# Kernel tuning notes

Measured on AMD Instinct MI355X. Metric: run time of the kernel, lower is better.

Reference implementation:

```python
import jax, jax.numpy as jnp
import numpy as np
from jax import lax

B, L, E, H, VOCAB = 32, 64, 1024, 128, 32000


def setup_inputs() -> dict:
    key = jax.random.key(0)
    ks = jax.random.split(key, 8)
    return {
        "sent": jax.random.randint(ks[0], (B, L), 0, VOCAB),
        "init_c": jax.random.normal(ks[1], (B, H), jnp.float32),
        "init_h": jax.random.normal(ks[2], (B, H), jnp.float32),
        "enc_output": jax.random.normal(ks[3], (B, E, H), jnp.float32),
        "w_emb": jax.random.normal(ks[4], (VOCAB, H), jnp.float32) * 0.02,
        "w_lstm": jax.random.normal(ks[5], (2 * H, 4 * H), jnp.float32) * 0.05,
        "w_soft": jax.random.normal(ks[6], (H, VOCAB), jnp.float32) * 0.05,
        "V": jax.random.normal(ks[7], (2 * H, H), jnp.float32) * 0.05,
    }


def reference(sent, init_c, init_h, enc_output, w_emb, w_lstm, w_soft, V):
    h_dim = init_h.shape[-1]
    x_emb = w_emb[sent]                       # (B, L, H) embedding lookup
    # Split additive-attention matrix: concat(enc, h) @ V == enc @ V_e + h @ V_h
    V_e, V_h = V[:h_dim], V[h_dim:]           # (H, H) each
    enc_proj = enc_output @ V_e               # (B, E, H), precomputed once

    def step(carry, x_t):
        c, h = carry
        # LSTM cell: gates from concat(x, h) @ w_lstm
        gates = jnp.concatenate([x_t, h], axis=-1) @ w_lstm   # (B, 4H)
        i, f, o, g = jnp.split(gates, 4, axis=-1)
        c_new = jax.nn.sigmoid(f) * c + jax.nn.sigmoid(i) * jnp.tanh(g)
        h_new = jax.nn.sigmoid(o) * jnp.tanh(c_new)           # (B, H)
        # Bahdanau additive attention over encoder states
        att = jnp.tanh(enc_proj + (h_new @ V_h)[:, None, :])  # (B, E, H)
        scores = att.sum(axis=-1)                              # (B, E)
        alpha = jax.nn.softmax(scores, axis=-1)                # (B, E)
        context = jnp.einsum('be,beh->bh', alpha, enc_output)  # (B, H)
        h_out = context                                        # attended hidden
        return (c_new, h_out), (h_out, alpha)

    (c_fin, h_fin), (hs, alphas) = lax.scan(step, (init_c, init_h),
                                            jnp.transpose(x_emb, (1, 0, 2)))
    hs = jnp.transpose(hs, (1, 0, 2))          # (B, L, H)
    alphas = jnp.transpose(alphas, (1, 0, 2))  # (B, L, E)
    logits = hs @ w_soft                       # (B, L, vocab)
    return logits, c_fin, h_fin, alphas
```

## Files before the change

### kernel.cpp

```cpp
#include <hip/hip_runtime.h>
#include <hip/hip_bf16.h>

#define BB 32
#define LL 64
#define EE 1024
#define HH 128
#define VV 32000

typedef unsigned short u16;
typedef unsigned long long u64;
typedef __attribute__((ext_vector_type(8))) short bf16x8;
typedef __attribute__((ext_vector_type(8))) unsigned short u16x8;
typedef __attribute__((ext_vector_type(4))) float f32x4;

#define LOG2E 1.4426950408889634f
#define C2T   2.8853900817779268f

#define OFF_C ((size_t)BB * LL * VV)
#define OFF_H (OFF_C + (size_t)BB * HH)
#define OFF_A (OFF_H + (size_t)BB * HH)

#define WS_ENCT 0
#define WS_HS   ((size_t)8388608)
#define WS_GX   ((size_t)8912896)
#define WS_PAYU ((size_t)13107200)
#define WS_PAYG ((size_t)13639680)
#define WS_WT   ((size_t)13901824)
#define WS_DFL  ((size_t)22093824)
#define WS_NEED ((size_t)22093828)

#define PAYU_WORDS (32 * 8 * 2 * 130)
#define PAYG_WORDS (32 * 8 * 2 * 64)
#define PAY_TOTAL  (PAYU_WORDS + PAYG_WORDS)

#define RESET_BLKS ((PAY_TOTAL + 255) / 256)
#define GX_BLKS    128
#define ENC_BLKS   (16 * BB)
#define TW_BLKS    ((VV / 32) * 4)
#define PREP_BLKS  (RESET_BLKS + GX_BLKS + ENC_BLKS + TW_BLKS)

__device__ __forceinline__ float bf2f(u16 u) {
    union { unsigned int i; float f; } v; v.i = ((unsigned int)u) << 16; return v.f;
}
__device__ __forceinline__ u16 f2bf(float f) {
    union { float f; unsigned int i; } v; v.f = f;
    unsigned int x = v.i;
    return (u16)((x + 0x7FFFu + ((x >> 16) & 1u)) >> 16);
}
__device__ __forceinline__ float ldf(const void* p, size_t i, int f32) {
    if (f32) return ((const float*)p)[i];
    return bf2f(((const u16*)p)[i]);
}
__device__ __forceinline__ void stout(void* p, size_t i, float v, int f32) {
    if (f32) ((float*)p)[i] = v;
    else ((u16*)p)[i] = f2bf(v);
}
__device__ __forceinline__ float sigm(float x) {
    return __builtin_amdgcn_rcpf(1.f + __builtin_amdgcn_exp2f(-x * LOG2E));
}
__device__ __forceinline__ float tanh_fast(float x) {
    return 1.f - 2.f * __builtin_amdgcn_rcpf(__builtin_amdgcn_exp2f(x * C2T) + 1.f);
}

__global__ __launch_bounds__(256) void megaprep_kernel(
    const int* __restrict__ sent, const void* __restrict__ w_emb,
    const void* __restrict__ w_lstm, const void* __restrict__ enc_out,
    const void* __restrict__ V, const void* __restrict__ w_soft,
    float* __restrict__ gx, u16* __restrict__ encT, u16* __restrict__ wT,
    u64* __restrict__ pay, int* __restrict__ flag)
{
    const int blk = blockIdx.x;
    const int tid = threadIdx.x;
    __shared__ float smem[16384];
    __shared__ int dcnt[4];

    if (blk < RESET_BLKS) {
        int i = blk * 256 + tid;
        if (i < PAY_TOTAL) pay[i] = 0ull;
        if (blk == 0) {
            float a = fabsf(bf2f((u16)(((const unsigned int*)w_emb)[tid] & 0xFFFFu)));
            unsigned long long m = __ballot(a > 1e-4f && a < 0.5f);
            if ((tid & 63) == 0) dcnt[tid >> 6] = __popcll(m);
            __syncthreads();
            if (tid == 0)
                *flag = (dcnt[0] + dcnt[1] + dcnt[2] + dcnt[3] > 128) ? 1 : 0;
        }
        return;
    }
    float da = fabsf(bf2f((u16)(((const unsigned int*)w_emb)[tid] & 0xFFFFu)));
    unsigned long long dm = __ballot(da > 1e-4f && da < 0.5f);
    if ((tid & 63) == 0) dcnt[tid >> 6] = __popcll(dm);
    __syncthreads();
    const int isf32 = !(dcnt[0] + dcnt[1] + dcnt[2] + dcnt[3] > 128);
    __syncthreads();

    if (blk < RESET_BLKS + GX_BLKS) {
        int row0 = (blk - RESET_BLKS) * 16;
        float (*xr)[128] = (float(*)[128])smem;
        for (int i = tid; i < 2048; i += 256) {
            int r = i >> 7, col = i & 127;
            int id = sent[row0 + r];
            xr[r][col] = ldf(w_emb, (size_t)id * HH + col, isf32);
        }
        __syncthreads();
        int c0 = tid, c1 = tid + 256;
        float a0[16], a1[16];
        #pragma unroll
        for (int r = 0; r < 16; ++r) { a0[r] = 0.f; a1[r] = 0.f; }
        for (int kk = 0; kk < 128; ++kk) {
            float w0, w1;
            if (isf32) {
                w0 = ((const float*)w_lstm)[(size_t)kk * 512 + c0];
                w1 = ((const float*)w_lstm)[(size_t)kk * 512 + c1];
            } else {
                w0 = bf2f(((const u16*)w_lstm)[(size_t)kk * 512 + c0]);
                w1 = bf2f(((const u16*)w_lstm)[(size_t)kk * 512 + c1]);
            }
            #pragma unroll
            for (int r = 0; r < 16; ++r) {
                a0[r] += xr[r][kk] * w0;
                a1[r] += xr[r][kk] * w1;
            }
        }
        #pragma unroll
        for (int r = 0; r < 16; ++r) {
            gx[(size_t)(row0 + r) * 512 + c0] = a0[r];
            gx[(size_t)(row0 + r) * 512 + c1] = a1[r];
        }
        return;
    }
    if (blk < RESET_BLKS + GX_BLKS + ENC_BLKS) {
        int idx = blk - RESET_BLKS - GX_BLKS;
        int b = idx >> 4;
        int e0 = (idx & 15) * 64;
        float (*ve)[128] = (float(*)[128])smem;
        for (int i = tid; i < HH * HH; i += 256)
            ve[i >> 7][i & 127] = ldf(V, i, isf32);
        __syncthreads();
        int e = e0 + (tid & 63);
        int hb = (tid >> 6) * 32;
        size_t rowbase = ((size_t)b * EE + e) * HH;
        float acc[32];
        #pragma unroll
        for (int i = 0; i < 32; ++i) acc[i] = 0.f;
        for (int k0 = 0; k0 < HH; k0 += 16) {
            float ef[16];
            #pragma unroll
            for (int i = 0; i < 16; ++i) ef[i] = ldf(enc_out, rowbase + k0 + i, isf32);
            #pragma unroll
            for (int hh = 0; hh < 32; ++hh) {
                float a = acc[hh];
                #pragma unroll
                for (int kk = 0; kk < 16; ++kk)
                    a += ef[kk] * ve[k0 + kk][hb + hh];
                acc[hh] = a;
            }
        }
        u16* outp = encT + ((size_t)b * HH) * EE + e;
        #pragma unroll
        for (int hh = 0; hh < 32; ++hh)
            outp[(size_t)(hh + hb) * EE] = f2bf(acc[hh] * C2T);
        return;
    }
    {
        int idx = blk - RESET_BLKS - GX_BLKS - ENC_BLKS;
        int n0 = (idx >> 2) * 32;
        int k0 = (idx & 3) * 32;
        u16 (*tile)[33] = (u16(*)[33])smem;
        int tx = tid & 31, ty0 = tid >> 5;
        #pragma unroll
        for (int i = 0; i < 4; ++i) {
            int ty = ty0 + i * 8;
            tile[ty][tx] = f2bf(ldf(w_soft, (size_t)(k0 + ty) * VV + n0 + tx, isf32));
        }
        __syncthreads();
        #pragma unroll
        for (int i = 0; i < 4; ++i) {
            int ty = ty0 + i * 8;
            wT[(size_t)(n0 + ty) * HH + k0 + tx] = tile[tx][ty];
        }
    }
}

__global__ __launch_bounds__(1024) void scan_kernel(
    const void* __restrict__ init_c, const void* __restrict__ init_h,
    const void* __restrict__ enc_out, const void* __restrict__ w_lstm,
    const void* __restrict__ V, const u16* __restrict__ encTg16,
    const float* __restrict__ gx, u16* __restrict__ hs_bf,
    void* __restrict__ out, u64* __restrict__ payu, u64* __restrict__ payg,
    const int* __restrict__ flagp)
{
    const int isf32 = !flagp[0];
    const int bid = blockIdx.x;
    const int b = bid & 31, k = bid >> 5;
    const int tid = threadIdx.x;

    __shared__ u16   encTl16[128][128];
    __shared__ float encF[128][128];
    __shared__ u16   wrec16[64 * 128];
    __shared__ float gall[512];
    __shared__ float harr[128], cst[128], hnew[128], hvC[128];
    __shared__ float dred[8][128];
    __shared__ float sc[128];
    __shared__ float exch[8][130];
    __shared__ float redw[2], redw2[2];
    __shared__ float m_s, s_s;

    for (int i = tid; i < 128 * 128; i += 1024) {
        int h = i >> 7, e = i & 127;
        encTl16[h][e] = encTg16[(size_t)(b * 128 + h) * EE + k * 128 + e];
    }
    for (int i = tid; i < 128 * 128; i += 1024) {
        int e = i >> 7, hh = i & 127;
        encF[e][hh] = ldf(enc_out, ((size_t)b * EE + k * 128 + e) * HH + hh, isf32);
    }
    for (int i = tid; i < 64 * 128; i += 1024) {
        int c = i >> 7, kk = i & 127;
        wrec16[c * 128 + kk] = f2bf(ldf(w_lstm, (size_t)(HH + kk) * 512 + k * 64 + c, isf32));
    }
    if (tid < 128) {
        cst[tid]  = ldf(init_c, (size_t)b * HH + tid, isf32);
        harr[tid] = ldf(init_h, (size_t)b * HH + tid, isf32);
    }
    __syncthreads();

    u64* mypu = payu + (size_t)(b * 8 + k) * 2 * 130;
    u64* mypg = payg + (size_t)(b * 8 + k) * 2 * 64;

    for (int t = 0; t < LL; ++t) {
        const unsigned int want = (unsigned int)(t + 1);
        float g0 = 0.f, g1 = 0.f, g2 = 0.f, g3 = 0.f;
        if (tid < 128) {
            const float* gxr = gx + (size_t)(b * LL + t) * 512;
            g0 = gxr[tid]; g1 = gxr[128 + tid]; g2 = gxr[256 + tid]; g3 = gxr[384 + tid];
        }
        {
            int colL = tid >> 4, kc = tid & 15;
            const bf16x8 wv = *(const bf16x8*)&wrec16[colL * 128 + kc * 8];
            float acc = 0.f;
            #pragma unroll
            for (int j = 0; j < 8; ++j)
                acc = __builtin_fmaf(harr[kc * 8 + j], bf2f((u16)wv[j]), acc);
            acc += __shfl_xor(acc, 1);
            acc += __shfl_xor(acc, 2);
            acc += __shfl_xor(acc, 4);
            acc += __shfl_xor(acc, 8);
            if (kc == 0) {
                gall[(k << 6) + colL] = acc;
                union { float f; unsigned int u; } cv; cv.f = acc;
                u64 w = ((u64)want << 32) | (u64)cv.u;
                __hip_atomic_store(&mypg[(size_t)(t & 1) * 64 + colL], w,
                                   __ATOMIC_RELAXED, __HIP_MEMORY_SCOPE_AGENT);
            }
        }
        if (tid < 448) {
            int qq = tid >> 6;
            int q = qq + (qq >= k ? 1 : 0);
            int idx = tid & 63;
            const u64* qp = payg + ((size_t)(b * 8 + q) * 2 + (t & 1)) * 64 + idx;
            u64 w = __hip_atomic_load(qp, __ATOMIC_RELAXED, __HIP_MEMORY_SCOPE_AGENT);
            int cnt = 0;
            while ((unsigned int)(w >> 32) != want) {
                __builtin_amdgcn_s_sleep(1);
                w = __hip_atomic_load(qp, __ATOMIC_RELAXED, __HIP_MEMORY_SCOPE_AGENT);
                if (++cnt > (1 << 20)) break;
            }
            union { unsigned int u; float f; } cv; cv.u = (unsigned int)(w & 0xFFFFFFFFu);
            gall[q * 64 + idx] = cv.f;
        }
        __syncthreads();
        if (tid < 128) {
            float gi = g0 + gall[tid];
            float gf = g1 + gall[128 + tid];
            float go = g2 + gall[256 + tid];
            float gg = g3 + gall[384 + tid];
            float c_new = sigm(gf) * cst[tid] + sigm(gi) * tanh_fast(gg);
            cst[tid] = c_new;
            hnew[tid] = sigm(go) * tanh_fast(c_new);
        }
        __syncthreads();
        {
            int h = tid & 127, jc = tid >> 7;
            float p = 0.f;
            if (isf32) {
                const float* vp = (const float*)V + (size_t)(HH + jc * 16) * HH + h;
                #pragma unroll
                for (int j = 0; j < 16; ++j)
                    p += hnew[jc * 16 + j] * vp[(size_t)j * HH];
            } else {
                const u16* vp = (const u16*)V + (size_t)(HH + jc * 16) * HH + h;
                #pragma unroll
                for (int j = 0; j < 16; ++j)
                    p += hnew[jc * 16 + j] * bf2f(vp[(size_t)j * HH]);
            }
            dred[jc][h] = p;
        }
        __syncthreads();
        if (tid < 128) {
            float v = 0.f;
            #pragma unroll
            for (int s = 0; s < 8; ++s) v += dred[s][tid];
            hvC[tid] = v * C2T;
        }
        __syncthreads();
        {
            int e = tid & 127, hc = tid >> 7;
            float sumr = 0.f;
            #pragma unroll
            for (int j = 0; j < 16; ++j) {
                int h = hc * 16 + j;
                float a = bf2f(encTl16[h][e]) + hvC[h];
                sumr += __builtin_amdgcn_rcpf(__builtin_amdgcn_exp2f(a) + 1.f);
            }
            dred[hc][e] = sumr;
        }
        __syncthreads();
        float s_e = 0.f, p_reg = 0.f;
        if (tid < 128) {
            float sr = 0.f;
            #pragma unroll
            for (int s = 0; s < 8; ++s) sr += dred[s][tid];
            s_e = 128.f - 2.f * sr;
            float m = s_e;
            #pragma unroll
            for (int off = 32; off; off >>= 1) m = fmaxf(m, __shfl_xor(m, off));
            if ((tid & 63) == 0) redw[tid >> 6] = m;
        }
        __syncthreads();
        if (tid < 128) {
            float mloc = fmaxf(redw[0], redw[1]);
            p_reg = __builtin_amdgcn_exp2f((s_e - mloc) * LOG2E);
            sc[tid] = p_reg;
            float s = p_reg;
            #pragma unroll
            for (int off = 32; off; off >>= 1) s += __shfl_xor(s, off);
            if ((tid & 63) == 0) redw2[tid >> 6] = s;
            if (tid == 0) m_s = mloc;
        }
        __syncthreads();
        if (tid == 0) s_s = redw2[0] + redw2[1];
        {
            int h = tid & 127, ec = tid >> 7;
            float p = 0.f;
            #pragma unroll
            for (int j = 0; j < 16; ++j)
                p += sc[ec * 16 + j] * encF[ec * 16 + j][h];
            dred[ec][h] = p;
        }
        __syncthreads();
        float Uv = 0.f;
        if (tid < 128) {
            #pragma unroll
            for (int s = 0; s < 8; ++s) Uv += dred[s][tid];
        }
        {
            u64* pp = mypu + (size_t)(t & 1) * 130;
            if (tid < 130) {
                float val = (tid < 128) ? Uv : ((tid == 128) ? m_s : s_s);
                union { float f; unsigned int u; } cv; cv.f = val;
                u64 w = ((u64)want << 32) | (u64)cv.u;
                __hip_atomic_store(&pp[tid], w, __ATOMIC_RELAXED, __HIP_MEMORY_SCOPE_AGENT);
                exch[k][tid] = val;
            }
        }
        if (tid < 910) {
            int qq = tid / 130;
            int q = qq + (qq >= k ? 1 : 0);
            int idx = tid - qq * 130;
            const u64* qp = payu + ((size_t)(b * 8 + q) * 2 + (t & 1)) * 130 + idx;
            u64 w = __hip_atomic_load(qp, __ATOMIC_RELAXED, __HIP_MEMORY_SCOPE_AGENT);
            int cnt = 0;
            while ((unsigned int)(w >> 32) != want) {
                __builtin_amdgcn_s_sleep(1);
                w = __hip_atomic_load(qp, __ATOMIC_RELAXED, __HIP_MEMORY_SCOPE_AGENT);
                if (++cnt > (1 << 20)) break;
            }
            union { unsigned int u; float f; } cv; cv.u = (unsigned int)(w & 0xFFFFFFFFu);
            exch[q][idx] = cv.f;
        }
        __syncthreads();
        if (tid < 128) {
            float M = exch[0][128];
            #pragma unroll
            for (int q = 1; q < 8; ++q) M = fmaxf(M, exch[q][128]);
            float St = 0.f, ch = 0.f;
            #pragma unroll
            for (int q = 0; q < 8; ++q) {
                float w = __builtin_amdgcn_exp2f((exch[q][128] - M) * LOG2E);
                St += w * exch[q][129];
                ch += w * exch[q][tid];
            }
            float rS = __builtin_amdgcn_rcpf(St);
            float ctx = ch * rS;
            harr[tid] = ctx;
            float al = p_reg * __builtin_amdgcn_exp2f((m_s - M) * LOG2E) * rS;
            stout(out, OFF_A + (size_t)(b * LL + t) * EE + k * 128 + tid, al, isf32);
            if (k == 0) {
                hs_bf[(size_t)(b * LL + t) * HH + tid] = f2bf(ctx);
                if (t == LL - 1) {
                    stout(out, OFF_H + (size_t)b * HH + tid, ctx, isf32);
                    stout(out, OFF_C + (size_t)b * HH + tid, cst[tid], isf32);
                }
            }
        }
        __syncthreads();
    }
}

__global__ __launch_bounds__(256) void logits_gemm(
    const u16* __restrict__ hs, const u16* __restrict__ wT,
    void* __restrict__ out, const int* __restrict__ flagp)
{
    int isf32 = !flagp[0];
    int n0 = blockIdx.x * 32;
    int m0 = (blockIdx.y * 4 + (threadIdx.x >> 6)) * 32;
    int lane = threadIdx.x & 63;
    int lr = lane & 15, lh = lane >> 4;
    f32x4 acc00 = {0.f, 0.f, 0.f, 0.f}, acc01 = acc00, acc10 = acc00, acc11 = acc00;
    const u16* a0p = hs + (size_t)(m0 + lr) * HH + lh * 8;
    const u16* a1p = a0p + (size_t)16 * HH;
    const u16* b0p = wT + (size_t)(n0 + lr) * HH + lh * 8;
    const u16* b1p = b0p + (size_t)16 * HH;
    #pragma unroll
    for (int ks = 0; ks < 4; ++ks) {
        bf16x8 a0 = *(const bf16x8*)(a0p + ks * 32);
        bf16x8 a1 = *(const bf16x8*)(a1p + ks * 32);
        bf16x8 b0 = *(const bf16x8*)(b0p + ks * 32);
        bf16x8 b1 = *(const bf16x8*)(b1p + ks * 32);
        acc00 = __builtin_amdgcn_mfma_f32_16x16x32_bf16(a0, b0, acc00, 0, 0, 0);
        acc01 = __builtin_amdgcn_mfma_f32_16x16x32_bf16(a0, b1, acc01, 0, 0, 0);
        acc10 = __builtin_amdgcn_mfma_f32_16x16x32_bf16(a1, b0, acc10, 0, 0, 0);
        acc11 = __builtin_amdgcn_mfma_f32_16x16x32_bf16(a1, b1, acc11, 0, 0, 0);
    }
    size_t base0 = (size_t)(m0 + lh * 4) * VV + n0;
    size_t base1 = (size_t)(m0 + 16 + lh * 4) * VV + n0;
    #pragma unroll
    for (int r = 0; r < 4; ++r) {
        stout(out, base0 + (size_t)r * VV + lr,      acc00[r], isf32);
        stout(out, base0 + (size_t)r * VV + 16 + lr, acc01[r], isf32);
        stout(out, base1 + (size_t)r * VV + lr,      acc10[r], isf32);
        stout(out, base1 + (size_t)r * VV + 16 + lr, acc11[r], isf32);
    }
}

extern "C" void kernel_launch(void* const* d_in, const int* in_sizes, int n_in,
                              void* d_out, int out_size, void* d_ws, size_t ws_size,
                              hipStream_t stream)
{
    (void)in_sizes; (void)n_in; (void)out_size;
    if (ws_size < WS_NEED) return;

    const int* sent     = (const int*)d_in[0];
    const void* init_c  = d_in[1];
    const void* init_h  = d_in[2];
    const void* enc_out = d_in[3];
    const void* w_emb   = d_in[4];
    const void* w_lstm  = d_in[5];
    const void* w_soft  = d_in[6];
    const void* V       = d_in[7];

    char* ws = (char*)d_ws;
    u16*   encT  = (u16*)(ws + WS_ENCT);
    u16*   hs    = (u16*)(ws + WS_HS);
    float* gx    = (float*)(ws + WS_GX);
    u64*   payu  = (u64*)(ws + WS_PAYU);
    u64*   payg  = (u64*)(ws + WS_PAYG);
    u16*   wT    = (u16*)(ws + WS_WT);
    int*   dflag = (int*)(ws + WS_DFL);

    hipLaunchKernelGGL(megaprep_kernel, dim3(PREP_BLKS), dim3(256), 0, stream,
                       sent, w_emb, w_lstm, enc_out, V, w_soft,
                       gx, encT, wT, payu, dflag);

    {
        const void* a0 = init_c; const void* a1 = init_h; const void* a2 = enc_out;
        const void* a3 = w_lstm; const void* a4 = V; const u16* a5 = encT;
        const float* a6 = gx; u16* a7 = hs; void* a8 = d_out;
        u64* a9 = payu; u64* a10 = payg; const int* a11 = dflag;
        void* args[] = {&a0, &a1, &a2, &a3, &a4, &a5, &a6, &a7, &a8, &a9, &a10, &a11};
        hipLaunchCooperativeKernel(scan_kernel, dim3(256), dim3(1024), args, 0, stream);
    }

    hipLaunchKernelGGL(logits_gemm, dim3(VV / 32, 16), dim3(256), 0, stream, hs, wT, d_out, dflag);
}
```

Baseline: 746.5 us.

## Fuse prep, scan and logits GEMM into one cooperative kernel

Merges the three launches (prep, recurrent scan, logits GEMM) into a single cooperative kernel that uses grid syncs between phases. The per-call transpose of w_soft into a bf16 workspace is dropped, and the GEMM phase reads w_soft directly with strided scalar loads and converts it in registers. Prep work (gx, the encoder projection, payload reset) is spread over the 256 persistent blocks. This removes launch gaps and a full pass over w_soft, but the GEMM now runs on only 256 blocks with uncoalesced B loads, and the prep phase has far less parallelism than before.

```diff
diff --git a/kernel.cpp b/kernel.cpp
--- a/kernel.cpp
+++ b/kernel.cpp
@@ -1,5 +1,8 @@
 #include <hip/hip_runtime.h>
 #include <hip/hip_bf16.h>
+#include <hip/hip_cooperative_groups.h>
+
+namespace cg = cooperative_groups;
 
 #define BB 32
 #define LL 64
@@ -25,19 +28,7 @@
 #define WS_GX   ((size_t)8912896)
 #define WS_PAYU ((size_t)13107200)
 #define WS_PAYG ((size_t)13639680)
-#define WS_WT   ((size_t)13901824)
-#define WS_DFL  ((size_t)22093824)
-#define WS_NEED ((size_t)22093828)
-
-#define PAYU_WORDS (32 * 8 * 2 * 130)
-#define PAYG_WORDS (32 * 8 * 2 * 64)
-#define PAY_TOTAL  (PAYU_WORDS + PAYG_WORDS)
-
-#define RESET_BLKS ((PAY_TOTAL + 255) / 256)
-#define GX_BLKS    128
-#define ENC_BLKS   (16 * BB)
-#define TW_BLKS    ((VV / 32) * 4)
-#define PREP_BLKS  (RESET_BLKS + GX_BLKS + ENC_BLKS + TW_BLKS)
+#define WS_NEED ((size_t)13901824)
 
 __device__ __forceinline__ float bf2f(u16 u) {
     union { unsigned int i; float f; } v; v.i = ((unsigned int)u) << 16; return v.f;
@@ -62,135 +53,14 @@
     return 1.f - 2.f * __builtin_amdgcn_rcpf(__builtin_amdgcn_exp2f(x * C2T) + 1.f);
 }
 
-__global__ __launch_bounds__(256) void megaprep_kernel(
+__global__ __launch_bounds__(1024) void fused_kernel(
     const int* __restrict__ sent, const void* __restrict__ w_emb,
     const void* __restrict__ w_lstm, const void* __restrict__ enc_out,
     const void* __restrict__ V, const void* __restrict__ w_soft,
-    float* __restrict__ gx, u16* __restrict__ encT, u16* __restrict__ wT,
-    u64* __restrict__ pay, int* __restrict__ flag)
+    const void* __restrict__ init_c, const void* __restrict__ init_h,
+    float* __restrict__ gx, u16* __restrict__ encTg16, u16* __restrict__ hs_bf,
+    void* __restrict__ out, u64* __restrict__ payu, u64* __restrict__ payg)
 {
-    const int blk = blockIdx.x;
-    const int tid = threadIdx.x;
-    __shared__ float smem[16384];
-    __shared__ int dcnt[4];
-
-    if (blk < RESET_BLKS) {
-        int i = blk * 256 + tid;
-        if (i < PAY_TOTAL) pay[i] = 0ull;
-        if (blk == 0) {
-            float a = fabsf(bf2f((u16)(((const unsigned int*)w_emb)[tid] & 0xFFFFu)));
-            unsigned long long m = __ballot(a > 1e-4f && a < 0.5f);
-            if ((tid & 63) == 0) dcnt[tid >> 6] = __popcll(m);
-            __syncthreads();
-            if (tid == 0)
-                *flag = (dcnt[0] + dcnt[1] + dcnt[2] + dcnt[3] > 128) ? 1 : 0;
-        }
-        return;
-    }
-    float da = fabsf(bf2f((u16)(((const unsigned int*)w_emb)[tid] & 0xFFFFu)));
-    unsigned long long dm = __ballot(da > 1e-4f && da < 0.5f);
-    if ((tid & 63) == 0) dcnt[tid >> 6] = __popcll(dm);
-    __syncthreads();
-    const int isf32 = !(dcnt[0] + dcnt[1] + dcnt[2] + dcnt[3] > 128);
-    __syncthreads();
-
-    if (blk < RESET_BLKS + GX_BLKS) {
-        int row0 = (blk - RESET_BLKS) * 16;
-        float (*xr)[128] = (float(*)[128])smem;
-        for (int i = tid; i < 2048; i += 256) {
-            int r = i >> 7, col = i & 127;
-            int id = sent[row0 + r];
-            xr[r][col] = ldf(w_emb, (size_t)id * HH + col, isf32);
-        }
-        __syncthreads();
-        int c0 = tid, c1 = tid + 256;
-        float a0[16], a1[16];
-        #pragma unroll
-        for (int r = 0; r < 16; ++r) { a0[r] = 0.f; a1[r] = 0.f; }
-        for (int kk = 0; kk < 128; ++kk) {
-            float w0, w1;
-            if (isf32) {
-                w0 = ((const float*)w_lstm)[(size_t)kk * 512 + c0];
-                w1 = ((const float*)w_lstm)[(size_t)kk * 512 + c1];
-            } else {
-                w0 = bf2f(((const u16*)w_lstm)[(size_t)kk * 512 + c0]);
-                w1 = bf2f(((const u16*)w_lstm)[(size_t)kk * 512 + c1]);
-            }
-            #pragma unroll
-            for (int r = 0; r < 16; ++r) {
-                a0[r] += xr[r][kk] * w0;
-                a1[r] += xr[r][kk] * w1;
-            }
-        }
-        #pragma unroll
-        for (int r = 0; r < 16; ++r) {
-            gx[(size_t)(row0 + r) * 512 + c0] = a0[r];
-            gx[(size_t)(row0 + r) * 512 + c1] = a1[r];
-        }
-        return;
-    }
-    if (blk < RESET_BLKS + GX_BLKS + ENC_BLKS) {
-        int idx = blk - RESET_BLKS - GX_BLKS;
-        int b = idx >> 4;
-        int e0 = (idx & 15) * 64;
-        float (*ve)[128] = (float(*)[128])smem;
-        for (int i = tid; i < HH * HH; i += 256)
-            ve[i >> 7][i & 127] = ldf(V, i, isf32);
-        __syncthreads();
-        int e = e0 + (tid & 63);
-        int hb = (tid >> 6) * 32;
-        size_t rowbase = ((size_t)b * EE + e) * HH;
-        float acc[32];
-        #pragma unroll
-        for (int i = 0; i < 32; ++i) acc[i] = 0.f;
-        for (int k0 = 0; k0 < HH; k0 += 16) {
-            float ef[16];
-            #pragma unroll
-            for (int i = 0; i < 16; ++i) ef[i] = ldf(enc_out, rowbase + k0 + i, isf32);
-            #pragma unroll
-            for (int hh = 0; hh < 32; ++hh) {
-                float a = acc[hh];
-                #pragma unroll
-                for (int kk = 0; kk < 16; ++kk)
-                    a += ef[kk] * ve[k0 + kk][hb + hh];
-                acc[hh] = a;
-            }
-        }
-        u16* outp = encT + ((size_t)b * HH) * EE + e;
-        #pragma unroll
-        for (int hh = 0; hh < 32; ++hh)
-            outp[(size_t)(hh + hb) * EE] = f2bf(acc[hh] * C2T);
-        return;
-    }
-    {
-        int idx = blk - RESET_BLKS - GX_BLKS - ENC_BLKS;
-        int n0 = (idx >> 2) * 32;
-        int k0 = (idx & 3) * 32;
-        u16 (*tile)[33] = (u16(*)[33])smem;
-        int tx = tid & 31, ty0 = tid >> 5;
-        #pragma unroll
-        for (int i = 0; i < 4; ++i) {
-            int ty = ty0 + i * 8;
-            tile[ty][tx] = f2bf(ldf(w_soft, (size_t)(k0 + ty) * VV + n0 + tx, isf32));
-        }
-        __syncthreads();
-        #pragma unroll
-        for (int i = 0; i < 4; ++i) {
-            int ty = ty0 + i * 8;
-            wT[(size_t)(n0 + ty) * HH + k0 + tx] = tile[tx][ty];
-        }
-    }
-}
-
-__global__ __launch_bounds__(1024) void scan_kernel(
-    const void* __restrict__ init_c, const void* __restrict__ init_h,
-    const void* __restrict__ enc_out, const void* __restrict__ w_lstm,
-    const void* __restrict__ V, const u16* __restrict__ encTg16,
-    const float* __restrict__ gx, u16* __restrict__ hs_bf,
-    void* __restrict__ out, u64* __restrict__ payu, u64* __restrict__ payg,
-    const int* __restrict__ flagp)
-{
-    const int isf32 = !flagp[0];
     const int bid = blockIdx.x;
     const int b = bid & 31, k = bid >> 5;
     const int tid = threadIdx.x;
@@ -205,6 +75,80 @@
     __shared__ float exch[8][130];
     __shared__ float redw[2], redw2[2];
     __shared__ float m_s, s_s;
+    __shared__ int dcnt[4];
+
+    if (tid < 256) {
+        float a = fabsf(bf2f((u16)(((const unsigned int*)w_emb)[tid] & 0xFFFFu)));
+        unsigned long long m = __ballot(a > 1e-4f && a < 0.5f);
+        if ((tid & 63) == 0) dcnt[tid >> 6] = __popcll(m);
+    }
+    __syncthreads();
+    const int isf32 = !(dcnt[0] + dcnt[1] + dcnt[2] + dcnt[3] > 128);
+
+    u64* mypu = payu + (size_t)(b * 8 + k) * 2 * 130;
+    u64* mypg = payg + (size_t)(b * 8 + k) * 2 * 64;
+    if (tid < 260) mypu[tid] = 0ull;
+    else if (tid < 260 + 128) mypg[tid - 260] = 0ull;
+
+    {
+        float (*xr)[128] = (float(*)[128])wrec16;
+        int row0 = bid * 8;
+        {
+            int r = tid >> 7, col = tid & 127;
+            int id = sent[row0 + r];
+            xr[r][col] = ldf(w_emb, (size_t)id * HH + col, isf32);
+        }
+        __syncthreads();
+        int c = tid & 511, rh = tid >> 9;
+        float a4[4] = {0.f, 0.f, 0.f, 0.f};
+        for (int kk = 0; kk < 128; ++kk) {
+            float wv = ldf(w_lstm, (size_t)kk * 512 + c, isf32);
+            #pragma unroll
+            for (int r = 0; r < 4; ++r)
+                a4[r] += xr[rh * 4 + r][kk] * wv;
+        }
+        #pragma unroll
+        for (int r = 0; r < 4; ++r)
+            gx[(size_t)(row0 + rh * 4 + r) * 512 + c] = a4[r];
+    }
+    __syncthreads();
+    {
+        float (*ve)[128] = (float(*)[128])encF;
+        for (int i = tid; i < HH * HH; i += 1024)
+            ve[i >> 7][i & 127] = ldf(V, i, isf32);
+        __syncthreads();
+        #pragma unroll
+        for (int u = 0; u < 2; ++u) {
+            int unit = bid * 2 + u;
+            int bb = unit >> 4;
+            int e0 = (unit & 15) * 64;
+            int e = e0 + (tid & 63);
+            int h0 = (tid >> 6) * 8;
+            size_t rowbase = ((size_t)bb * EE + e) * HH;
+            float acc[8];
+            #pragma unroll
+            for (int i = 0; i < 8; ++i) acc[i] = 0.f;
+            for (int k0 = 0; k0 < HH; k0 += 16) {
+                float ef[16];
+                #pragma unroll
+                for (int i = 0; i < 16; ++i) ef[i] = ldf(enc_out, rowbase + k0 + i, isf32);
+                #pragma unroll
+                for (int hh = 0; hh < 8; ++hh) {
+                    float a = acc[hh];
+                    #pragma unroll
+                    for (int kk = 0; kk < 16; ++kk)
+                        a += ef[kk] * ve[k0 + kk][h0 + hh];
+                    acc[hh] = a;
+                }
+            }
+            u16* outp = encTg16 + ((size_t)bb * HH) * EE + e;
+            #pragma unroll
+            for (int hh = 0; hh < 8; ++hh)
+                outp[(size_t)(h0 + hh) * EE] = f2bf(acc[hh] * C2T);
+        }
+    }
+    __threadfence();
+    cg::this_grid().sync();
 
     for (int i = tid; i < 128 * 128; i += 1024) {
         int h = i >> 7, e = i & 127;
@@ -223,9 +167,6 @@
         harr[tid] = ldf(init_h, (size_t)b * HH + tid, isf32);
     }
     __syncthreads();
-
-    u64* mypu = payu + (size_t)(b * 8 + k) * 2 * 130;
-    u64* mypg = payg + (size_t)(b * 8 + k) * 2 * 64;
 
     for (int t = 0; t < LL; ++t) {
         const unsigned int want = (unsigned int)(t + 1);
@@ -405,41 +346,46 @@
         }
         __syncthreads();
     }
-}
-
-__global__ __launch_bounds__(256) void logits_gemm(
-    const u16* __restrict__ hs, const u16* __restrict__ wT,
-    void* __restrict__ out, const int* __restrict__ flagp)
-{
-    int isf32 = !flagp[0];
-    int n0 = blockIdx.x * 32;
-    int m0 = (blockIdx.y * 4 + (threadIdx.x >> 6)) * 32;
-    int lane = threadIdx.x & 63;
-    int lr = lane & 15, lh = lane >> 4;
-    f32x4 acc00 = {0.f, 0.f, 0.f, 0.f}, acc01 = acc00, acc10 = acc00, acc11 = acc00;
-    const u16* a0p = hs + (size_t)(m0 + lr) * HH + lh * 8;
-    const u16* a1p = a0p + (size_t)16 * HH;
-    const u16* b0p = wT + (size_t)(n0 + lr) * HH + lh * 8;
-    const u16* b1p = b0p + (size_t)16 * HH;
-    #pragma unroll
-    for (int ks = 0; ks < 4; ++ks) {
-        bf16x8 a0 = *(const bf16x8*)(a0p + ks * 32);
-        bf16x8 a1 = *(const bf16x8*)(a1p + ks * 32);
-        bf16x8 b0 = *(const bf16x8*)(b0p + ks * 32);
-        bf16x8 b1 = *(const bf16x8*)(b1p + ks * 32);
-        acc00 = __builtin_amdgcn_mfma_f32_16x16x32_bf16(a0, b0, acc00, 0, 0, 0);
-        acc01 = __builtin_amdgcn_mfma_f32_16x16x32_bf16(a0, b1, acc01, 0, 0, 0);
-        acc10 = __builtin_amdgcn_mfma_f32_16x16x32_bf16(a1, b0, acc10, 0, 0, 0);
-        acc11 = __builtin_amdgcn_mfma_f32_16x16x32_bf16(a1, b1, acc11, 0, 0, 0);
-    }
-    size_t base0 = (size_t)(m0 + lh * 4) * VV + n0;
-    size_t base1 = (size_t)(m0 + 16 + lh * 4) * VV + n0;
-    #pragma unroll
-    for (int r = 0; r < 4; ++r) {
-        stout(out, base0 + (size_t)r * VV + lr,      acc00[r], isf32);
-        stout(out, base0 + (size_t)r * VV + 16 + lr, acc01[r], isf32);
-        stout(out, base1 + (size_t)r * VV + lr,      acc10[r], isf32);
-        stout(out, base1 + (size_t)r * VV + 16 + lr, acc11[r], isf32);
+
+    __threadfence();
+    cg::this_grid().sync();
+
+    {
+        const int wgl = bid * 16 + (tid >> 6);
+        const int lane = tid & 63;
+        const int lr = lane & 15, lh = lane >> 4;
+        for (int task = wgl; task < 64000; task += 4096) {
+            int nx = task >> 6, my = task & 63;
+            int n0 = nx * 32, m0 = my * 32;
+            f32x4 acc00 = {0.f, 0.f, 0.f, 0.f}, acc01 = acc00, acc10 = acc00, acc11 = acc00;
+            const u16* a0p = hs_bf + (size_t)(m0 + lr) * HH + lh * 8;
+            const u16* a1p = a0p + (size_t)16 * HH;
+            #pragma unroll
+            for (int ks = 0; ks < 4; ++ks) {
+                bf16x8 a0 = *(const bf16x8*)(a0p + ks * 32);
+                bf16x8 a1 = *(const bf16x8*)(a1p + ks * 32);
+                bf16x8 b0, b1;
+                #pragma unroll
+                for (int j = 0; j < 8; ++j) {
+                    int kk = ks * 32 + lh * 8 + j;
+                    b0[j] = (short)f2bf(ldf(w_soft, (size_t)kk * VV + n0 + lr, isf32));
+                    b1[j] = (short)f2bf(ldf(w_soft, (size_t)kk * VV + n0 + 16 + lr, isf32));
+                }
+                acc00 = __builtin_amdgcn_mfma_f32_16x16x32_bf16(a0, b0, acc00, 0, 0, 0);
+                acc01 = __builtin_amdgcn_mfma_f32_16x16x32_bf16(a0, b1, acc01, 0, 0, 0);
+                acc10 = __builtin_amdgcn_mfma_f32_16x16x32_bf16(a1, b0, acc10, 0, 0, 0);
+                acc11 = __builtin_amdgcn_mfma_f32_16x16x32_bf16(a1, b1, acc11, 0, 0, 0);
+            }
+            size_t base0 = (size_t)(m0 + lh * 4) * VV + n0;
+            size_t base1 = (size_t)(m0 + 16 + lh * 4) * VV + n0;
+            #pragma unroll
+            for (int r = 0; r < 4; ++r) {
+                stout(out, base0 + (size_t)r * VV + lr,      acc00[r], isf32);
+                stout(out, base0 + (size_t)r * VV + 16 + lr, acc01[r], isf32);
+                stout(out, base1 + (size_t)r * VV + lr,      acc10[r], isf32);
+                stout(out, base1 + (size_t)r * VV + 16 + lr, acc11[r], isf32);
+            }
+        }
     }
 }
 
@@ -465,21 +411,13 @@
     float* gx    = (float*)(ws + WS_GX);
     u64*   payu  = (u64*)(ws + WS_PAYU);
     u64*   payg  = (u64*)(ws + WS_PAYG);
-    u16*   wT    = (u16*)(ws + WS_WT);
-    int*   dflag = (int*)(ws + WS_DFL);
-
-    hipLaunchKernelGGL(megaprep_kernel, dim3(PREP_BLKS), dim3(256), 0, stream,
-                       sent, w_emb, w_lstm, enc_out, V, w_soft,
-                       gx, encT, wT, payu, dflag);
-
-    {
-        const void* a0 = init_c; const void* a1 = init_h; const void* a2 = enc_out;
-        const void* a3 = w_lstm; const void* a4 = V; const u16* a5 = encT;
-        const float* a6 = gx; u16* a7 = hs; void* a8 = d_out;
-        u64* a9 = payu; u64* a10 = payg; const int* a11 = dflag;
-        void* args[] = {&a0, &a1, &a2, &a3, &a4, &a5, &a6, &a7, &a8, &a9, &a10, &a11};
-        hipLaunchCooperativeKernel(scan_kernel, dim3(256), dim3(1024), args, 0, stream);
-    }
-
-    hipLaunchKernelGGL(logits_gemm, dim3(VV / 32, 16), dim3(256), 0, stream, hs, wT, d_out, dflag);
-}
+
+    const int* a0 = sent; const void* a1 = w_emb; const void* a2 = w_lstm;
+    const void* a3 = enc_out; const void* a4 = V; const void* a5 = w_soft;
+    const void* a6 = init_c; const void* a7 = init_h;
+    float* a8 = gx; u16* a9 = encT; u16* a10 = hs; void* a11 = d_out;
+    u64* a12 = payu; u64* a13 = payg;
+    void* args[] = {&a0, &a1, &a2, &a3, &a4, &a5, &a6, &a7,
+                    &a8, &a9, &a10, &a11, &a12, &a13};
+    hipLaunchCooperativeKernel(fused_kernel, dim3(256), dim3(1024), args, 0, stream);
+}
```

Result: slower. 979.1 us (+31.2%).

## Fuse logits GEMM into cooperative scan kernel after grid sync

Applied to the files above, without the earlier changes.

Moves the output-projection GEMM into the tail of the cooperative scan kernel, separated by a grid-wide barrier, with each wave looping over 32x32 output tiles. This removes one kernel launch and the gap between launches. In exchange, the GEMM runs with only 256 blocks of 1024 threads, limited by the scan kernel's occupancy and its heavy shared-memory use, instead of a large grid that can fully occupy the GPU.

```diff
diff --git a/kernel.cpp b/kernel.cpp
--- a/kernel.cpp
+++ b/kernel.cpp
@@ -1,5 +1,8 @@
 #include <hip/hip_runtime.h>
 #include <hip/hip_bf16.h>
+#include <hip/hip_cooperative_groups.h>
+
+namespace cg = cooperative_groups;
 
 #define BB 32
 #define LL 64
@@ -182,13 +185,13 @@
     }
 }
 
-__global__ __launch_bounds__(1024) void scan_kernel(
+__global__ __launch_bounds__(1024) void scan_logits_kernel(
     const void* __restrict__ init_c, const void* __restrict__ init_h,
     const void* __restrict__ enc_out, const void* __restrict__ w_lstm,
     const void* __restrict__ V, const u16* __restrict__ encTg16,
     const float* __restrict__ gx, u16* __restrict__ hs_bf,
     void* __restrict__ out, u64* __restrict__ payu, u64* __restrict__ payg,
-    const int* __restrict__ flagp)
+    const u16* __restrict__ wT, const int* __restrict__ flagp)
 {
     const int isf32 = !flagp[0];
     const int bid = blockIdx.x;
@@ -405,41 +408,43 @@
         }
         __syncthreads();
     }
-}
-
-__global__ __launch_bounds__(256) void logits_gemm(
-    const u16* __restrict__ hs, const u16* __restrict__ wT,
-    void* __restrict__ out, const int* __restrict__ flagp)
-{
-    int isf32 = !flagp[0];
-    int n0 = blockIdx.x * 32;
-    int m0 = (blockIdx.y * 4 + (threadIdx.x >> 6)) * 32;
-    int lane = threadIdx.x & 63;
-    int lr = lane & 15, lh = lane >> 4;
-    f32x4 acc00 = {0.f, 0.f, 0.f, 0.f}, acc01 = acc00, acc10 = acc00, acc11 = acc00;
-    const u16* a0p = hs + (size_t)(m0 + lr) * HH + lh * 8;
-    const u16* a1p = a0p + (size_t)16 * HH;
-    const u16* b0p = wT + (size_t)(n0 + lr) * HH + lh * 8;
-    const u16* b1p = b0p + (size_t)16 * HH;
-    #pragma unroll
-    for (int ks = 0; ks < 4; ++ks) {
-        bf16x8 a0 = *(const bf16x8*)(a0p + ks * 32);
-        bf16x8 a1 = *(const bf16x8*)(a1p + ks * 32);
-        bf16x8 b0 = *(const bf16x8*)(b0p + ks * 32);
-        bf16x8 b1 = *(const bf16x8*)(b1p + ks * 32);
-        acc00 = __builtin_amdgcn_mfma_f32_16x16x32_bf16(a0, b0, acc00, 0, 0, 0);
-        acc01 = __builtin_amdgcn_mfma_f32_16x16x32_bf16(a0, b1, acc01, 0, 0, 0);
-        acc10 = __builtin_amdgcn_mfma_f32_16x16x32_bf16(a1, b0, acc10, 0, 0, 0);
-        acc11 = __builtin_amdgcn_mfma_f32_16x16x32_bf16(a1, b1, acc11, 0, 0, 0);
-    }
-    size_t base0 = (size_t)(m0 + lh * 4) * VV + n0;
-    size_t base1 = (size_t)(m0 + 16 + lh * 4) * VV + n0;
-    #pragma unroll
-    for (int r = 0; r < 4; ++r) {
-        stout(out, base0 + (size_t)r * VV + lr,      acc00[r], isf32);
-        stout(out, base0 + (size_t)r * VV + 16 + lr, acc01[r], isf32);
-        stout(out, base1 + (size_t)r * VV + lr,      acc10[r], isf32);
-        stout(out, base1 + (size_t)r * VV + 16 + lr, acc11[r], isf32);
+
+    __threadfence();
+    cg::this_grid().sync();
+
+    {
+        const int wgl = bid * 16 + (tid >> 6);
+        const int lane = tid & 63;
+        const int lr = lane & 15, lh = lane >> 4;
+        for (int task = wgl; task < 64000; task += 4096) {
+            int nx = task >> 6, my = task & 63;
+            int n0 = nx * 32, m0 = my * 32;
+            f32x4 acc00 = {0.f, 0.f, 0.f, 0.f}, acc01 = acc00, acc10 = acc00, acc11 = acc00;
+            const u16* a0p = hs_bf + (size_t)(m0 + lr) * HH + lh * 8;
+            const u16* a1p = a0p + (size_t)16 * HH;
+            const u16* b0p = wT + (size_t)(n0 + lr) * HH + lh * 8;
+            const u16* b1p = b0p + (size_t)16 * HH;
+            #pragma unroll
+            for (int ks = 0; ks < 4; ++ks) {
+                bf16x8 a0 = *(const bf16x8*)(a0p + ks * 32);
+                bf16x8 a1 = *(const bf16x8*)(a1p + ks * 32);
+                bf16x8 b0 = *(const bf16x8*)(b0p + ks * 32);
+                bf16x8 b1 = *(const bf16x8*)(b1p + ks * 32);
+                acc00 = __builtin_amdgcn_mfma_f32_16x16x32_bf16(a0, b0, acc00, 0, 0, 0);
+                acc01 = __builtin_amdgcn_mfma_f32_16x16x32_bf16(a0, b1, acc01, 0, 0, 0);
+                acc10 = __builtin_amdgcn_mfma_f32_16x16x32_bf16(a1, b0, acc10, 0, 0, 0);
+                acc11 = __builtin_amdgcn_mfma_f32_16x16x32_bf16(a1, b1, acc11, 0, 0, 0);
+            }
+            size_t base0 = (size_t)(m0 + lh * 4) * VV + n0;
+            size_t base1 = (size_t)(m0 + 16 + lh * 4) * VV + n0;
+            #pragma unroll
+            for (int r = 0; r < 4; ++r) {
+                stout(out, base0 + (size_t)r * VV + lr,      acc00[r], isf32);
+                stout(out, base0 + (size_t)r * VV + 16 + lr, acc01[r], isf32);
+                stout(out, base1 + (size_t)r * VV + lr,      acc10[r], isf32);
+                stout(out, base1 + (size_t)r * VV + 16 + lr, acc11[r], isf32);
+            }
+        }
     }
 }
 
@@ -476,10 +481,8 @@
         const void* a0 = init_c; const void* a1 = init_h; const void* a2 = enc_out;
         const void* a3 = w_lstm; const void* a4 = V; const u16* a5 = encT;
         const float* a6 = gx; u16* a7 = hs; void* a8 = d_out;
-        u64* a9 = payu; u64* a10 = payg; const int* a11 = dflag;
-        void* args[] = {&a0, &a1, &a2, &a3, &a4, &a5, &a6, &a7, &a8, &a9, &a10, &a11};
-        hipLaunchCooperativeKernel(scan_kernel, dim3(256), dim3(1024), args, 0, stream);
-    }
-
-    hipLaunchKernelGGL(logits_gemm, dim3(VV / 32, 16), dim3(256), 0, stream, hs, wT, d_out, dflag);
-}
+        u64* a9 = payu; u64* a10 = payg; const u16* a11 = wT; const int* a12 = dflag;
+        void* args[] = {&a0, &a1, &a2, &a3, &a4, &a5, &a6, &a7, &a8, &a9, &a10, &a11, &a12};
+        hipLaunchCooperativeKernel(scan_logits_kernel, dim3(256), dim3(1024), args, 0, stream);
+    }
+}
```

Result: slower. 813.4 us (+9.0%).
